# Performance work log

Hardware: AMD Instinct MI355X
Metric: run time of the kernel (lower is better)

The kernel has to match this reference:

```python
import jax, jax.numpy as jnp
import numpy as np

N, E, D_IN, D_OUT = 16384, 4096, 256, 256


def _leaky(v):
    return jnp.where(v > 0, v, 0.1 * v)


def setup_inputs() -> dict:
    key = jax.random.key(0)
    ks = jax.random.split(key, 8)
    x = jax.random.normal(ks[0], (N, D_IN), dtype=jnp.float32)
    # 0/1 incidence mask, float32 (as multiplied in the torch code)
    H_shape = jax.random.randint(ks[1], (N, E), 0, 2).astype(jnp.float32)
    w1 = jax.random.normal(ks[2], (D_IN, D_OUT), dtype=jnp.float32)
    w2 = jax.random.normal(ks[3], (D_OUT, D_OUT), dtype=jnp.float32)
    a1 = jax.random.normal(ks[4], (D_OUT, 1), dtype=jnp.float32)
    a21 = jax.random.normal(ks[5], (D_OUT, 1), dtype=jnp.float32)
    a22 = jax.random.normal(ks[6], (D_OUT, 1), dtype=jnp.float32)
    return {"x": x, "H_shape": H_shape, "w1": w1, "w2": w2,
            "a1": a1, "a21": a21, "a22": a22}


def reference(x, H_shape, w1, w2, a1, a21, a22):
    xw1 = x @ w1                                  # [N, D]
    # node->edge attention (masked softmax-like over nodes, axis -2)
    f = _leaky(xw1) @ a1                          # [N, 1]
    e = jnp.exp(jnp.tanh(f / 8) * 8) * H_shape    # [N, E]
    e = e / jnp.sum(e, axis=-2, keepdims=True)    # normalize over nodes
    # edge features
    f = _leaky(e.T @ xw1)                         # [E, D]
    # edge->node attention (masked normalize over edges, axis -1)
    b = (_leaky(f @ w2) @ a21).T + _leaky(xw1) @ a22  # [1,E] + [N,1] -> [N,E]
    b = jnp.exp(jnp.tanh(b / 8) * 8) * H_shape
    b = b / jnp.sum(b, axis=-1, keepdims=True)
    return _leaky(b @ f @ w2)                     # [N, D]
```

## Files before the change

### kernel.cpp

```cpp
#include <hip/hip_runtime.h>


typedef __attribute__((ext_vector_type(8))) short short8;
typedef __attribute__((ext_vector_type(4))) float f32x4;
typedef __attribute__((ext_vector_type(4))) int int4v;
typedef __attribute__((ext_vector_type(4))) unsigned int uint4v;

__device__ __forceinline__ float leakyf(float v) { return v > 0.f ? v : 0.1f * v; }
__device__ __forceinline__ float fastrcp(float x) { return __builtin_amdgcn_rcpf(x); }

__device__ __forceinline__ float satexpf(float t) {
    float u = fminf(fmaxf(t * 0.25f, -30.f), 30.f);
    float p = __expf(u);
    float th = (p - 1.f) * fastrcp(p + 1.f);
    return __expf(8.f * th);
}

__device__ __forceinline__ short f2b(float v) {
    unsigned int x = __float_as_uint(v);
    x += 0x7fffu + ((x >> 16) & 1u);
    return (short)(x >> 16);
}
__device__ __forceinline__ float b2f(short s) {
    return __uint_as_float(((unsigned int)(unsigned short)s) << 16);
}

__global__ __launch_bounds__(256) void transpose_split2(
        const float* __restrict__ s0, short* __restrict__ dh0, short* __restrict__ dl0,
        const float* __restrict__ s1, short* __restrict__ dh1, short* __restrict__ dl1) {
    const float* src = blockIdx.z ? s1 : s0;
    short* dh = blockIdx.z ? dh1 : dh0;
    short* dl = blockIdx.z ? dl1 : dl0;
    __shared__ float Ts[64][65];
    const int t = threadIdx.x;
    const long r0 = (long)blockIdx.x * 64;
    const long c0 = (long)blockIdx.y * 64;
    {
        const int row = t >> 2, cc = (t & 3) * 16;
        const float* p = src + (r0 + row) * 256 + c0 + cc;
#pragma unroll
        for (int i = 0; i < 4; ++i) {
            f32x4 v = *reinterpret_cast<const f32x4*>(p + i * 4);
#pragma unroll
            for (int k = 0; k < 4; ++k) Ts[row][cc + i * 4 + k] = v[k];
        }
    }
    __syncthreads();
    {
        const int cl = t >> 2, ch = (t & 3) * 16;
        short8 h0, h1, l0, l1;
#pragma unroll
        for (int i = 0; i < 8; ++i) {
            float v = Ts[ch + i][cl];
            short h = f2b(v);
            h0[i] = h; l0[i] = f2b(v - b2f(h));
        }
#pragma unroll
        for (int i = 0; i < 8; ++i) {
            float v = Ts[ch + 8 + i][cl];
            short h = f2b(v);
            h1[i] = h; l1[i] = f2b(v - b2f(h));
        }
        short* qh = dh + (c0 + cl) * 256 + r0 + ch;
        short* ql = dl + (c0 + cl) * 256 + r0 + ch;
        *reinterpret_cast<short8*>(qh) = h0;
        *reinterpret_cast<short8*>(qh + 8) = h1;
        *reinterpret_cast<short8*>(ql) = l0;
        *reinterpret_cast<short8*>(ql + 8) = l1;
    }
}

__global__ __launch_bounds__(256) void transposeH_pack(
        const float* __restrict__ H, char* __restrict__ HbT,
        unsigned int* __restrict__ Hbits) {
    __shared__ float Ts[64][65];
    const int t = threadIdx.x;
    const long r0 = (long)blockIdx.x * 64;
    const long c0 = (long)blockIdx.y * 64;
    {
        const int row = t >> 2, cc = (t & 3) * 16;
        const float* p = H + (r0 + row) * 4096L + c0 + cc;
#pragma unroll
        for (int i = 0; i < 4; ++i) {
            f32x4 v = *reinterpret_cast<const f32x4*>(p + i * 4);
#pragma unroll
            for (int k = 0; k < 4; ++k) Ts[row][cc + i * 4 + k] = v[k];
        }
    }
    __syncthreads();
    {
        const int cl = t >> 2, ch = (t & 3) * 16;
        uint4v pk;
#pragma unroll
        for (int wv = 0; wv < 4; ++wv) {
            unsigned int u = 0;
#pragma unroll
            for (int b = 0; b < 4; ++b)
                u |= (Ts[ch + wv * 4 + b][cl] != 0.f ? 1u : 0u) << (8 * b);
            pk[wv] = u;
        }
        *reinterpret_cast<uint4v*>(HbT + (c0 + cl) * 16384L + r0 + ch) = pk;
    }
    if (t < 128) {
        const int nl = t >> 1, w = t & 1;
        unsigned int u = 0;
#pragma unroll
        for (int b = 0; b < 32; ++b)
            u |= (Ts[nl][w * 32 + b] != 0.f ? 1u : 0u) << b;
        Hbits[(r0 + nl) * 128 + (c0 >> 5) + w] = u;
    }
}

__global__ __launch_bounds__(256) void gemm_xw1(
        const float* __restrict__ A, const short* __restrict__ Bh,
        const short* __restrict__ Bl, float* __restrict__ C) {
    __shared__ short Ash[128][72];
    __shared__ short Asl[128][72];
    __shared__ short Bsh[64][72];
    __shared__ short Bsl[64][72];
    const int t = threadIdx.x;
    const int wid = t >> 6, lane = t & 63;
    const int wm = wid & 1, wn = wid >> 1;
    const int quad = lane >> 4, l15 = lane & 15;
    const long m0 = (long)blockIdx.x * 128;
    const long n0 = (long)blockIdx.y * 64;
    f32x4 acc[4][2];
#pragma unroll
    for (int i = 0; i < 4; ++i)
#pragma unroll
        for (int j = 0; j < 2; ++j)
#pragma unroll
            for (int r = 0; r < 4; ++r) acc[i][j][r] = 0.f;

    for (int kb = 0; kb < 256; kb += 64) {
#pragma unroll
        for (int it = 0; it < 4; ++it) {
            const int cid = t + it * 256;
            const int row = cid >> 3, c8 = (cid & 7) * 8;
            const float* ap = A + (m0 + row) * 256 + kb + c8;
            f32x4 v0 = *reinterpret_cast<const f32x4*>(ap);
            f32x4 v1 = *reinterpret_cast<const f32x4*>(ap + 4);
            short8 hi, lo;
#pragma unroll
            for (int k = 0; k < 4; ++k) {
                short h0 = f2b(v0[k]); hi[k] = h0; lo[k] = f2b(v0[k] - b2f(h0));
                short h1 = f2b(v1[k]); hi[4 + k] = h1; lo[4 + k] = f2b(v1[k] - b2f(h1));
            }
            *reinterpret_cast<short8*>(&Ash[row][c8]) = hi;
            *reinterpret_cast<short8*>(&Asl[row][c8]) = lo;
        }
#pragma unroll
        for (int it = 0; it < 2; ++it) {
            const int cid = t + it * 256;
            const int row = cid >> 3, c8 = (cid & 7) * 8;
            *reinterpret_cast<short8*>(&Bsh[row][c8]) =
                *reinterpret_cast<const short8*>(Bh + (n0 + row) * 256 + kb + c8);
            *reinterpret_cast<short8*>(&Bsl[row][c8]) =
                *reinterpret_cast<const short8*>(Bl + (n0 + row) * 256 + kb + c8);
        }
        __syncthreads();
#pragma unroll
        for (int ks = 0; ks < 2; ++ks) {
            short8 ah[4], al[4], bh[2], bl[2];
#pragma unroll
            for (int i = 0; i < 4; ++i) {
                ah[i] = *reinterpret_cast<const short8*>(&Ash[wm * 64 + i * 16 + l15][ks * 32 + quad * 8]);
                al[i] = *reinterpret_cast<const short8*>(&Asl[wm * 64 + i * 16 + l15][ks * 32 + quad * 8]);
            }
#pragma unroll
            for (int j = 0; j < 2; ++j) {
                bh[j] = *reinterpret_cast<const short8*>(&Bsh[wn * 32 + j * 16 + l15][ks * 32 + quad * 8]);
                bl[j] = *reinterpret_cast<const short8*>(&Bsl[wn * 32 + j * 16 + l15][ks * 32 + quad * 8]);
            }
#pragma unroll
            for (int i = 0; i < 4; ++i)
#pragma unroll
                for (int j = 0; j < 2; ++j) {
                    acc[i][j] = __builtin_amdgcn_mfma_f32_16x16x32_bf16(ah[i], bh[j], acc[i][j], 0, 0, 0);
                    acc[i][j] = __builtin_amdgcn_mfma_f32_16x16x32_bf16(ah[i], bl[j], acc[i][j], 0, 0, 0);
                    acc[i][j] = __builtin_amdgcn_mfma_f32_16x16x32_bf16(al[i], bh[j], acc[i][j], 0, 0, 0);
                }
        }
        __syncthreads();
    }
#pragma unroll
    for (int i = 0; i < 4; ++i) {
        const long grow = m0 + wm * 64 + i * 16 + quad * 4;
#pragma unroll
        for (int j = 0; j < 2; ++j) {
            const long gcol = n0 + wn * 32 + j * 16 + l15;
#pragma unroll
            for (int r = 0; r < 4; ++r)
                C[(grow + r) * 256 + gcol] = acc[i][j][r];
        }
    }
}

__global__ __launch_bounds__(256) void node_stats1(
        const float* __restrict__ xw1, const float* __restrict__ a1,
        const float* __restrict__ a22, float* __restrict__ g_out,
        float* __restrict__ dn, unsigned int* __restrict__ ddmax) {
    __shared__ float Mx[4][260];
    const int t = threadIdx.x;
    const int n0 = blockIdx.x * 64;
    const int r = t >> 2, q = t & 3;
    const long n = n0 + r;
    const float* xp = xw1 + n * 256 + q * 64;
    float vals[64];
    float facc = 0.f, dacc = 0.f;
#pragma unroll
    for (int i = 0; i < 16; ++i) {
        f32x4 v  = *reinterpret_cast<const f32x4*>(xp + i * 4);
        f32x4 b1 = *reinterpret_cast<const f32x4*>(a1 + q * 64 + i * 4);
        f32x4 b2 = *reinterpret_cast<const f32x4*>(a22 + q * 64 + i * 4);
#pragma unroll
        for (int k = 0; k < 4; ++k) {
            float lv = leakyf(v[k]);
            facc += lv * b1[k];
            dacc += lv * b2[k];
            vals[i * 4 + k] = v[k];
        }
    }
    facc += __shfl_xor(facc, 1); facc += __shfl_xor(facc, 2);
    dacc += __shfl_xor(dacc, 1); dacc += __shfl_xor(dacc, 2);
    const float g = satexpf(facc);
    if (q == 0) { dn[n] = dacc; g_out[n] = g; }
    float lm[64];
#pragma unroll
    for (int i = 0; i < 64; ++i) lm[i] = fabsf(vals[i] * g);
#pragma unroll
    for (int m = 4; m < 64; m <<= 1)
#pragma unroll
        for (int i = 0; i < 64; ++i) lm[i] = fmaxf(lm[i], __shfl_xor(lm[i], m));
    float gm = g;
#pragma unroll
    for (int m = 1; m < 64; m <<= 1) gm = fmaxf(gm, __shfl_xor(gm, m));
    const int wv = t >> 6, lane = t & 63;
    if (lane < 4) {
#pragma unroll
        for (int i = 0; i < 64; ++i) Mx[wv][lane * 64 + i] = lm[i];
    }
    if (lane == 0) Mx[wv][256] = gm;
    __syncthreads();
    if (t < 256) {
        float m = fmaxf(fmaxf(Mx[0][t], Mx[1][t]), fmaxf(Mx[2][t], Mx[3][t]));
        atomicMax(&ddmax[t], __float_as_uint(m));
    }
    if (t == 0) {
        float m = fmaxf(fmaxf(Mx[0][256], Mx[1][256]), fmaxf(Mx[2][256], Mx[3][256]));
        atomicMax(&ddmax[256], __float_as_uint(m));
    }
}

__global__ __launch_bounds__(256) void quantize_y(
        const float* __restrict__ xw1, const float* __restrict__ g_in,
        const unsigned int* __restrict__ ddmax, char* __restrict__ yQ) {
    __shared__ unsigned int Qh[257][16];
    __shared__ unsigned int Ql[257][16];
    const int t = threadIdx.x;
    const int n0 = blockIdx.x * 64;
    const int dd0 = (t >> 4) * 16;
    const int w = t & 15;
    const int r4 = w * 4;
    float s[16];
#pragma unroll
    for (int i = 0; i < 16; ++i)
        s[i] = 32512.f / __uint_as_float(ddmax[dd0 + i]);
    const float sg = 32512.f / __uint_as_float(ddmax[256]);
    unsigned int bh[16], bl[16];
#pragma unroll
    for (int i = 0; i < 16; ++i) { bh[i] = 0u; bl[i] = 0u; }
    unsigned int gh = 0u, gl = 0u;
#pragma unroll
    for (int rr = 0; rr < 4; ++rr) {
        const long n = n0 + r4 + rr;
        const float gg = g_in[n];
        const float* xp = xw1 + n * 256 + dd0;
#pragma unroll
        for (int c = 0; c < 4; ++c) {
            f32x4 v = *reinterpret_cast<const f32x4*>(xp + c * 4);
#pragma unroll
            for (int k = 0; k < 4; ++k) {
                const int i = c * 4 + k;
                int qv = __float2int_rn(v[k] * gg * s[i]);
                qv = max(-32639, min(32639, qv));
                const int qh = (qv + 128) >> 8;
                const int ql = qv - (qh << 8);
                bh[i] |= ((unsigned int)(qh & 255)) << (8 * rr);
                bl[i] |= ((unsigned int)(ql & 255)) << (8 * rr);
            }
        }
        if (t < 16) {
            int qv = __float2int_rn(gg * sg);
            qv = max(-32639, min(32639, qv));
            const int qh = (qv + 128) >> 8;
            const int ql = qv - (qh << 8);
            gh |= ((unsigned int)(qh & 255)) << (8 * rr);
            gl |= ((unsigned int)(ql & 255)) << (8 * rr);
        }
    }
#pragma unroll
    for (int i = 0; i < 16; ++i) { Qh[dd0 + i][w] = bh[i]; Ql[dd0 + i][w] = bl[i]; }
    if (t < 16) { Qh[256][t] = gh; Ql[256][t] = gl; }
    __syncthreads();
#pragma unroll
    for (int it = 0; it < 2; ++it) {
        const int dd = it * 256 + t;
        if (dd < 288) {
#pragma unroll
            for (int s2 = 0; s2 < 4; ++s2) {
                uint4v vh, vl;
                if (dd < 257) {
                    vh = *reinterpret_cast<const uint4v*>(&Qh[dd][s2 * 4]);
                    vl = *reinterpret_cast<const uint4v*>(&Ql[dd][s2 * 4]);
                } else {
#pragma unroll
                    for (int k = 0; k < 4; ++k) { vh[k] = 0u; vl[k] = 0u; }
                }
                *reinterpret_cast<uint4v*>(yQ + (long)dd * 16384 + n0 + s2 * 16) = vh;
                *reinterpret_cast<uint4v*>(yQ + (long)(288 + dd) * 16384 + n0 + s2 * 16) = vl;
            }
        }
    }
}

__global__ __launch_bounds__(256) void gemm_c1_i8(
        const char* __restrict__ Ab, const char* __restrict__ Bb,
        float* __restrict__ Cp) {
    __shared__ char As[128][144];
    __shared__ char Bsh[96][144];
    __shared__ char Bsl[96][144];
    const int t = threadIdx.x;
    const int wid = t >> 6, lane = t & 63;
    const int wm = wid & 1, wn = wid >> 1;
    const int quad = lane >> 4, l15 = lane & 15;
    const long m0 = (long)blockIdx.x * 128;
    const long n0 = (long)blockIdx.y * 96;
    const long k0 = (long)blockIdx.z * 2048;
    float* Cz = Cp + (long)blockIdx.z * (4096L * 288);
    int4v acch[4][3], accl[4][3];
#pragma unroll
    for (int i = 0; i < 4; ++i)
#pragma unroll
        for (int j = 0; j < 3; ++j)
#pragma unroll
            for (int r = 0; r < 4; ++r) { acch[i][j][r] = 0; accl[i][j][r] = 0; }

    for (int kb = 0; kb < 2048; kb += 128) {
#pragma unroll
        for (int it = 0; it < 4; ++it) {
            const int cid = t + it * 256;
            const int row = cid >> 3, seg = (cid & 7) * 16;
            *reinterpret_cast<uint4v*>(&As[row][seg]) =
                *reinterpret_cast<const uint4v*>(Ab + (m0 + row) * 16384 + k0 + kb + seg);
        }
#pragma unroll
        for (int it = 0; it < 3; ++it) {
            const int cid = t + it * 256;
            const int row = cid >> 3, seg = (cid & 7) * 16;
            *reinterpret_cast<uint4v*>(&Bsh[row][seg]) =
                *reinterpret_cast<const uint4v*>(Bb + (n0 + row) * 16384 + k0 + kb + seg);
            *reinterpret_cast<uint4v*>(&Bsl[row][seg]) =
                *reinterpret_cast<const uint4v*>(Bb + (288 + n0 + row) * 16384 + k0 + kb + seg);
        }
        __syncthreads();
#pragma unroll
        for (int ks = 0; ks < 2; ++ks) {
            int4v af[4], bh[3], bl[3];
#pragma unroll
            for (int i = 0; i < 4; ++i)
                af[i] = *reinterpret_cast<const int4v*>(
                        &As[wm * 64 + i * 16 + l15][ks * 64 + quad * 16]);
#pragma unroll
            for (int j = 0; j < 3; ++j) {
                bh[j] = *reinterpret_cast<const int4v*>(
                        &Bsh[wn * 48 + j * 16 + l15][ks * 64 + quad * 16]);
                bl[j] = *reinterpret_cast<const int4v*>(
                        &Bsl[wn * 48 + j * 16 + l15][ks * 64 + quad * 16]);
            }
#pragma unroll
            for (int i = 0; i < 4; ++i)
#pragma unroll
                for (int j = 0; j < 3; ++j) {
                    acch[i][j] = __builtin_amdgcn_mfma_i32_16x16x64_i8(af[i], bh[j], acch[i][j], 0, 0, 0);
                    accl[i][j] = __builtin_amdgcn_mfma_i32_16x16x64_i8(af[i], bl[j], accl[i][j], 0, 0, 0);
                }
        }
        __syncthreads();
    }
#pragma unroll
    for (int i = 0; i < 4; ++i) {
        const long grow = m0 + wm * 64 + i * 16 + quad * 4;
#pragma unroll
        for (int j = 0; j < 3; ++j) {
            const long gcol = n0 + wn * 48 + j * 16 + l15;
#pragma unroll
            for (int r = 0; r < 4; ++r)
                Cz[(grow + r) * 288 + gcol] =
                    256.f * (float)acch[i][j][r] + (float)accl[i][j][r];
        }
    }
}

__global__ __launch_bounds__(256) void reduce_C1(
        const float* __restrict__ C1p, const unsigned int* __restrict__ ddmax,
        float* __restrict__ C1) {
    const int i = blockIdx.x * 256 + threadIdx.x;
    const int dd = i % 288;
    float s = 0.f;
#pragma unroll
    for (int z = 0; z < 8; ++z) s += C1p[(long)z * 4096 * 288 + i];
    C1[i] = s * (__uint_as_float(ddmax[dd]) * (1.f / 32512.f));
}

__global__ __launch_bounds__(256) void gemm_G(
        const float* __restrict__ C1, const short* __restrict__ w2Th,
        const short* __restrict__ w2Tl, const float* __restrict__ a21,
        short* __restrict__ GT, float* __restrict__ cat) {
    __shared__ short Ash[64][72];
    __shared__ short Asl[64][72];
    __shared__ short Bsh[64][72];
    __shared__ short Bsl[64][72];
    __shared__ float Gs[64][65];
    const int t = threadIdx.x;
    const int wid = t >> 6, lane = t & 63;
    const int wm = wid & 1, wn = wid >> 1;
    const int quad = lane >> 4, l15 = lane & 15;
    const long j0 = (long)blockIdx.x * 64;
    const long d0 = (long)blockIdx.y * 64;
    f32x4 acc[2][2];
#pragma unroll
    for (int i = 0; i < 2; ++i)
#pragma unroll
        for (int j = 0; j < 2; ++j)
#pragma unroll
            for (int r = 0; r < 4; ++r) acc[i][j][r] = 0.f;

    for (int kb = 0; kb < 256; kb += 64) {
#pragma unroll
        for (int it = 0; it < 2; ++it) {
            const int cid = t + it * 256;
            const int row = cid >> 3, c8 = (cid & 7) * 8;
            const float rd = fastrcp(C1[(j0 + row) * 288 + 256]);
            const float* ap = C1 + (j0 + row) * 288 + kb + c8;
            f32x4 v0 = *reinterpret_cast<const f32x4*>(ap);
            f32x4 v1 = *reinterpret_cast<const f32x4*>(ap + 4);
            short8 hi, lo;
#pragma unroll
            for (int k = 0; k < 4; ++k) {
                float f0 = leakyf(v0[k] * rd);
                float f1 = leakyf(v1[k] * rd);
                short h0 = f2b(f0); hi[k] = h0; lo[k] = f2b(f0 - b2f(h0));
                short h1 = f2b(f1); hi[4 + k] = h1; lo[4 + k] = f2b(f1 - b2f(h1));
            }
            *reinterpret_cast<short8*>(&Ash[row][c8]) = hi;
            *reinterpret_cast<short8*>(&Asl[row][c8]) = lo;
            *reinterpret_cast<short8*>(&Bsh[row][c8]) =
                *reinterpret_cast<const short8*>(w2Th + (d0 + row) * 256 + kb + c8);
            *reinterpret_cast<short8*>(&Bsl[row][c8]) =
                *reinterpret_cast<const short8*>(w2Tl + (d0 + row) * 256 + kb + c8);
        }
        __syncthreads();
#pragma unroll
        for (int ks = 0; ks < 2; ++ks) {
            short8 ah[2], al[2], bh[2], bl[2];
#pragma unroll
            for (int i = 0; i < 2; ++i) {
                ah[i] = *reinterpret_cast<const short8*>(&Ash[wm * 32 + i * 16 + l15][ks * 32 + quad * 8]);
                al[i] = *reinterpret_cast<const short8*>(&Asl[wm * 32 + i * 16 + l15][ks * 32 + quad * 8]);
            }
#pragma unroll
            for (int j = 0; j < 2; ++j) {
                bh[j] = *reinterpret_cast<const short8*>(&Bsh[wn * 32 + j * 16 + l15][ks * 32 + quad * 8]);
                bl[j] = *reinterpret_cast<const short8*>(&Bsl[wn * 32 + j * 16 + l15][ks * 32 + quad * 8]);
            }
#pragma unroll
            for (int i = 0; i < 2; ++i)
#pragma unroll
                for (int j = 0; j < 2; ++j) {
                    acc[i][j] = __builtin_amdgcn_mfma_f32_16x16x32_bf16(ah[i], bh[j], acc[i][j], 0, 0, 0);
                    acc[i][j] = __builtin_amdgcn_mfma_f32_16x16x32_bf16(ah[i], bl[j], acc[i][j], 0, 0, 0);
                    acc[i][j] = __builtin_amdgcn_mfma_f32_16x16x32_bf16(al[i], bh[j], acc[i][j], 0, 0, 0);
                }
        }
        __syncthreads();
    }
#pragma unroll
    for (int i = 0; i < 2; ++i)
#pragma unroll
        for (int j = 0; j < 2; ++j)
#pragma unroll
            for (int r = 0; r < 4; ++r)
                Gs[wm * 32 + i * 16 + quad * 4 + r][wn * 32 + j * 16 + l15] = acc[i][j][r];
    __syncthreads();
    {
        const int jl = t >> 2, q = t & 3;
        float cp = 0.f;
#pragma unroll
        for (int i = 0; i < 16; ++i) {
            const int d = q * 16 + i;
            cp += leakyf(Gs[jl][d]) * a21[d0 + d];
        }
        cp += __shfl_xor(cp, 1); cp += __shfl_xor(cp, 2);
        if (q == 0) atomicAdd(&cat[j0 + jl], cp);
    }
    {
        const int dl = t >> 2, q = t & 3;
        short8 pk0, pk1;
#pragma unroll
        for (int i = 0; i < 8; ++i) pk0[i] = f2b(Gs[q * 16 + i][dl]);
#pragma unroll
        for (int i = 0; i < 8; ++i) pk1[i] = f2b(Gs[q * 16 + 8 + i][dl]);
        short* gp = GT + (d0 + dl) * 4096 + j0 + q * 16;
        *reinterpret_cast<short8*>(gp) = pk0;
        *reinterpret_cast<short8*>(gp + 8) = pk1;
    }
}

__global__ __launch_bounds__(256) void fused_out(
        const unsigned int* __restrict__ Hbits, const float* __restrict__ cat,
        const float* __restrict__ dn, const short* __restrict__ GT,
        float* __restrict__ out) {
    __shared__ float catS[4096];
    __shared__ unsigned int bitsS[64][132];
    __shared__ short As[64][72];
    __shared__ short Bs[256][72];
    __shared__ float rsS[64][4];
    __shared__ float rinvS[64];
    const int t = threadIdx.x;
    const int wid = t >> 6, lane = t & 63;
    const int wm = wid & 1, wn = wid >> 1;
    const int quad = lane >> 4, l15 = lane & 15;
    const long m0 = (long)blockIdx.x * 64;
    const int r = t & 63, jc = t >> 6;
    const float drow = dn[m0 + r];

#pragma unroll
    for (int i = 0; i < 4; ++i) {
        f32x4 v = *reinterpret_cast<const f32x4*>(cat + t * 16 + i * 4);
        *reinterpret_cast<f32x4*>(&catS[t * 16 + i * 4]) = v;
    }
#pragma unroll
    for (int it = 0; it < 8; ++it) {
        const int cid = t + it * 256;
        const int row = cid >> 5, ch = (cid & 31) * 4;
        *reinterpret_cast<uint4v*>(&bitsS[row][ch]) =
            *reinterpret_cast<const uint4v*>(Hbits + (m0 + row) * 128 + ch);
    }

    f32x4 acc[2][8];
#pragma unroll
    for (int i = 0; i < 2; ++i)
#pragma unroll
        for (int j = 0; j < 8; ++j)
#pragma unroll
            for (int x = 0; x < 4; ++x) acc[i][j][x] = 0.f;
    float racc = 0.f;
    __syncthreads();

    for (int kb = 0; kb < 4096; kb += 64) {
#pragma unroll
        for (int it = 0; it < 8; ++it) {
            const int cid = t + it * 256;
            const int row = cid >> 3, c8 = (cid & 7) * 8;
            *reinterpret_cast<short8*>(&Bs[row][c8]) =
                *reinterpret_cast<const short8*>(GT + row * 4096 + kb + c8);
        }
        {
            const unsigned int w = bitsS[r][(kb >> 5) + (jc >> 1)];
            const int bo = (jc & 1) * 16;
            short8 pk0, pk1;
#pragma unroll
            for (int c = 0; c < 4; ++c) {
                f32x4 cv = *reinterpret_cast<const f32x4*>(&catS[kb + jc * 16 + c * 4]);
#pragma unroll
                for (int k = 0; k < 4; ++k) {
                    const int kk = c * 4 + k;
                    const float s = ((w >> (bo + kk)) & 1u) ? satexpf(cv[k] + drow) : 0.f;
                    const short sb = f2b(s);
                    if (kk < 8) pk0[kk] = sb; else pk1[kk - 8] = sb;
                    racc += b2f(sb);
                }
            }
            *reinterpret_cast<short8*>(&As[r][jc * 16]) = pk0;
            *reinterpret_cast<short8*>(&As[r][jc * 16 + 8]) = pk1;
        }
        __syncthreads();
#pragma unroll
        for (int ks = 0; ks < 2; ++ks) {
            short8 af[2], bf[8];
#pragma unroll
            for (int i = 0; i < 2; ++i)
                af[i] = *reinterpret_cast<const short8*>(
                        &As[wm * 32 + i * 16 + l15][ks * 32 + quad * 8]);
#pragma unroll
            for (int j = 0; j < 8; ++j)
                bf[j] = *reinterpret_cast<const short8*>(
                        &Bs[wn * 128 + j * 16 + l15][ks * 32 + quad * 8]);
#pragma unroll
            for (int i = 0; i < 2; ++i)
#pragma unroll
                for (int j = 0; j < 8; ++j)
                    acc[i][j] = __builtin_amdgcn_mfma_f32_16x16x32_bf16(
                            af[i], bf[j], acc[i][j], 0, 0, 0);
        }
        __syncthreads();
    }
    rsS[r][jc] = racc;
    __syncthreads();
    if (t < 64)
        rinvS[t] = fastrcp(rsS[t][0] + rsS[t][1] + rsS[t][2] + rsS[t][3]);
    __syncthreads();
#pragma unroll
    for (int i = 0; i < 2; ++i) {
#pragma unroll
        for (int j = 0; j < 8; ++j) {
            const long gcol = wn * 128 + j * 16 + l15;
#pragma unroll
            for (int x = 0; x < 4; ++x) {
                const int rl = wm * 32 + i * 16 + quad * 4 + x;
                out[(m0 + rl) * 256 + gcol] = leakyf(acc[i][j][x] * rinvS[rl]);
            }
        }
    }
}

extern "C" void kernel_launch(void* const* d_in, const int* in_sizes, int n_in,
                              void* d_out, int out_size, void* d_ws, size_t ws_size,
                              hipStream_t stream) {
    const float* x   = (const float*)d_in[0];
    const float* H   = (const float*)d_in[1];
    const float* w1  = (const float*)d_in[2];
    const float* w2  = (const float*)d_in[3];
    const float* a1  = (const float*)d_in[4];
    const float* a21 = (const float*)d_in[5];
    const float* a22 = (const float*)d_in[6];
    float* out = (float*)d_out;
    char* ws = (char*)d_ws;

    float* xw1   = (float*)(ws + 0);
    float* C1p   = (float*)(ws + 0);
    char*  HbT   = (char*)(ws + 67108864);
    char*  yQ    = (char*)(ws + 134217728);
    float* dn    = (float*)(ws + 143654912);
    float* g     = (float*)(ws + 143720448);
    unsigned int* ddmax = (unsigned int*)(ws + 143785984);
    short* w1Th  = (short*)(ws + 143790080);
    short* w1Tl  = (short*)(ws + 143921152);
    short* w2Th  = (short*)(ws + 144052224);
    short* w2Tl  = (short*)(ws + 144183296);
    float* C1    = (float*)(ws + 144314368);
    short* GT    = (short*)(ws + 149032960);
    float* cat   = (float*)(ws + 151130112);
    unsigned int* Hbits = (unsigned int*)(ws + 151212032);

    hipMemsetAsync(ddmax, 0, 288 * sizeof(unsigned int), stream);
    hipMemsetAsync(cat, 0, 4096 * sizeof(float), stream);

    transpose_split2<<<dim3(4, 4, 2), 256, 0, stream>>>(
            w1, w1Th, w1Tl, w2, w2Th, w2Tl);
    transposeH_pack<<<dim3(256, 64), 256, 0, stream>>>(H, HbT, Hbits);

    gemm_xw1<<<dim3(128, 4), 256, 0, stream>>>(x, w1Th, w1Tl, xw1);
    node_stats1<<<dim3(256), 256, 0, stream>>>(xw1, a1, a22, g, dn, ddmax);
    quantize_y<<<dim3(256), 256, 0, stream>>>(xw1, g, ddmax, yQ);

    gemm_c1_i8<<<dim3(32, 3, 8), 256, 0, stream>>>(HbT, yQ, C1p);
    reduce_C1<<<dim3(4608), 256, 0, stream>>>(C1p, ddmax, C1);

    gemm_G<<<dim3(64, 4), 256, 0, stream>>>(C1, w2Th, w2Tl, a21, GT, cat);

    fused_out<<<dim3(256), 256, 0, stream>>>(Hbits, cat, dn, GT, out);
}
```

Baseline: 682.5 us.

## Store transposed incidence as bits and expand to int8 in C1 GEMM; widen fused_out

The transpose kernel now writes a bit-packed transposed incidence matrix instead of the 64 MB byte matrix. The int8 C1 GEMM reads these bits and expands them to 0/1 bytes in shared memory with a multiply-mask trick. It also changes the tile shape to 256x48 with split-K of 4, which halves the partial-sum reduction. fused_out moves to 512 threads, drops the shared cat and bits staging, and reads cat and bit words directly from global memory. This cuts the incidence write and read traffic by 8x, in exchange for extra ALU work on bit expansion and fewer parallel blocks in the C1 GEMM.

Result: no change. 675.6 us (-1.0%).

```diff
diff --git a/kernel.cpp b/kernel.cpp
--- a/kernel.cpp
+++ b/kernel.cpp
@@ -23,6 +23,9 @@
 }
 __device__ __forceinline__ float b2f(short s) {
     return __uint_as_float(((unsigned int)(unsigned short)s) << 16);
+}
+__device__ __forceinline__ unsigned int bits4_to_bytes(unsigned int s) {
+    return ((s & 0xFu) * 0x00204081u) & 0x01010101u;
 }
 
 __global__ __launch_bounds__(256) void transpose_split2(
@@ -71,8 +74,8 @@
 }
 
 __global__ __launch_bounds__(256) void transposeH_pack(
-        const float* __restrict__ H, char* __restrict__ HbT,
-        unsigned int* __restrict__ Hbits) {
+        const float* __restrict__ H, unsigned int* __restrict__ Hbits,
+        unsigned int* __restrict__ HbitsT) {
     __shared__ float Ts[64][65];
     const int t = threadIdx.x;
     const long r0 = (long)blockIdx.x * 64;
@@ -88,19 +91,6 @@
         }
     }
     __syncthreads();
-    {
-        const int cl = t >> 2, ch = (t & 3) * 16;
-        uint4v pk;
-#pragma unroll
-        for (int wv = 0; wv < 4; ++wv) {
-            unsigned int u = 0;
-#pragma unroll
-            for (int b = 0; b < 4; ++b)
-                u |= (Ts[ch + wv * 4 + b][cl] != 0.f ? 1u : 0u) << (8 * b);
-            pk[wv] = u;
-        }
-        *reinterpret_cast<uint4v*>(HbT + (c0 + cl) * 16384L + r0 + ch) = pk;
-    }
     if (t < 128) {
         const int nl = t >> 1, w = t & 1;
         unsigned int u = 0;
@@ -108,6 +98,14 @@
         for (int b = 0; b < 32; ++b)
             u |= (Ts[nl][w * 32 + b] != 0.f ? 1u : 0u) << b;
         Hbits[(r0 + nl) * 128 + (c0 >> 5) + w] = u;
+    } else {
+        const int t2 = t - 128;
+        const int jl = t2 >> 1, w = t2 & 1;
+        unsigned int u = 0;
+#pragma unroll
+        for (int b = 0; b < 32; ++b)
+            u |= (Ts[w * 32 + b][jl] != 0.f ? 1u : 0u) << b;
+        HbitsT[(c0 + jl) * 512 + (r0 >> 5) + w] = u;
     }
 }
 
@@ -324,19 +322,18 @@
     }
 }
 
-__global__ __launch_bounds__(256) void gemm_c1_i8(
-        const char* __restrict__ Ab, const char* __restrict__ Bb,
+__global__ __launch_bounds__(256) void gemm_c1_bits(
+        const unsigned int* __restrict__ HbitsT, const char* __restrict__ Bb,
         float* __restrict__ Cp) {
-    __shared__ char As[128][144];
-    __shared__ char Bsh[96][144];
-    __shared__ char Bsl[96][144];
+    __shared__ char As[256][144];
+    __shared__ char Bsh[48][144];
+    __shared__ char Bsl[48][144];
     const int t = threadIdx.x;
     const int wid = t >> 6, lane = t & 63;
-    const int wm = wid & 1, wn = wid >> 1;
     const int quad = lane >> 4, l15 = lane & 15;
-    const long m0 = (long)blockIdx.x * 128;
-    const long n0 = (long)blockIdx.y * 96;
-    const long k0 = (long)blockIdx.z * 2048;
+    const long m0 = (long)blockIdx.x * 256;
+    const long n0 = (long)blockIdx.y * 48;
+    const long k0 = (long)blockIdx.z * 4096;
     float* Cz = Cp + (long)blockIdx.z * (4096L * 288);
     int4v acch[4][3], accl[4][3];
 #pragma unroll
@@ -346,22 +343,31 @@
 #pragma unroll
             for (int r = 0; r < 4; ++r) { acch[i][j][r] = 0; accl[i][j][r] = 0; }
 
-    for (int kb = 0; kb < 2048; kb += 128) {
-#pragma unroll
-        for (int it = 0; it < 4; ++it) {
-            const int cid = t + it * 256;
-            const int row = cid >> 3, seg = (cid & 7) * 16;
-            *reinterpret_cast<uint4v*>(&As[row][seg]) =
-                *reinterpret_cast<const uint4v*>(Ab + (m0 + row) * 16384 + k0 + kb + seg);
+    for (int kb = 0; kb < 4096; kb += 128) {
+        {
+            uint4v bv = *reinterpret_cast<const uint4v*>(
+                    HbitsT + (m0 + t) * 512 + ((k0 + kb) >> 5));
+#pragma unroll
+            for (int w4 = 0; w4 < 4; ++w4) {
+                const unsigned int u = bv[w4];
+                uint4v e0, e1;
+#pragma unroll
+                for (int k = 0; k < 4; ++k) e0[k] = bits4_to_bytes(u >> (4 * k));
+#pragma unroll
+                for (int k = 0; k < 4; ++k) e1[k] = bits4_to_bytes(u >> (16 + 4 * k));
+                *reinterpret_cast<uint4v*>(&As[t][w4 * 32]) = e0;
+                *reinterpret_cast<uint4v*>(&As[t][w4 * 32 + 16]) = e1;
+            }
         }
 #pragma unroll
         for (int it = 0; it < 3; ++it) {
             const int cid = t + it * 256;
-            const int row = cid >> 3, seg = (cid & 7) * 16;
-            *reinterpret_cast<uint4v*>(&Bsh[row][seg]) =
-                *reinterpret_cast<const uint4v*>(Bb + (n0 + row) * 16384 + k0 + kb + seg);
-            *reinterpret_cast<uint4v*>(&Bsl[row][seg]) =
-                *reinterpret_cast<const uint4v*>(Bb + (288 + n0 + row) * 16384 + k0 + kb + seg);
+            const int idx = (cid < 384) ? cid : cid - 384;
+            const int row = idx >> 3, seg = (idx & 7) * 16;
+            char* dst = (cid >= 384) ? &Bsl[row][seg] : &Bsh[row][seg];
+            const long srow = (cid >= 384) ? (288 + n0 + row) : (n0 + row);
+            *reinterpret_cast<uint4v*>(dst) =
+                *reinterpret_cast<const uint4v*>(Bb + srow * 16384 + k0 + kb + seg);
         }
         __syncthreads();
 #pragma unroll
@@ -370,13 +376,11 @@
 #pragma unroll
             for (int i = 0; i < 4; ++i)
                 af[i] = *reinterpret_cast<const int4v*>(
-                        &As[wm * 64 + i * 16 + l15][ks * 64 + quad * 16]);
+                        &As[wid * 64 + i * 16 + l15][ks * 64 + quad * 16]);
 #pragma unroll
             for (int j = 0; j < 3; ++j) {
-                bh[j] = *reinterpret_cast<const int4v*>(
-                        &Bsh[wn * 48 + j * 16 + l15][ks * 64 + quad * 16]);
-                bl[j] = *reinterpret_cast<const int4v*>(
-                        &Bsl[wn * 48 + j * 16 + l15][ks * 64 + quad * 16]);
+                bh[j] = *reinterpret_cast<const int4v*>(&Bsh[j * 16 + l15][ks * 64 + quad * 16]);
+                bl[j] = *reinterpret_cast<const int4v*>(&Bsl[j * 16 + l15][ks * 64 + quad * 16]);
             }
 #pragma unroll
             for (int i = 0; i < 4; ++i)
@@ -390,10 +394,10 @@
     }
 #pragma unroll
     for (int i = 0; i < 4; ++i) {
-        const long grow = m0 + wm * 64 + i * 16 + quad * 4;
+        const long grow = m0 + wid * 64 + i * 16 + quad * 4;
 #pragma unroll
         for (int j = 0; j < 3; ++j) {
-            const long gcol = n0 + wn * 48 + j * 16 + l15;
+            const long gcol = n0 + j * 16 + l15;
 #pragma unroll
             for (int r = 0; r < 4; ++r)
                 Cz[(grow + r) * 288 + gcol] =
@@ -409,7 +413,7 @@
     const int dd = i % 288;
     float s = 0.f;
 #pragma unroll
-    for (int z = 0; z < 8; ++z) s += C1p[(long)z * 4096 * 288 + i];
+    for (int z = 0; z < 4; ++z) s += C1p[(long)z * 4096 * 288 + i];
     C1[i] = s * (__uint_as_float(ddmax[dd]) * (1.f / 32512.f));
 }
 
@@ -517,105 +521,97 @@
     }
 }
 
-__global__ __launch_bounds__(256) void fused_out(
+__global__ __launch_bounds__(512) void fused_out(
         const unsigned int* __restrict__ Hbits, const float* __restrict__ cat,
         const float* __restrict__ dn, const short* __restrict__ GT,
         float* __restrict__ out) {
-    __shared__ float catS[4096];
-    __shared__ unsigned int bitsS[64][132];
     __shared__ short As[64][72];
     __shared__ short Bs[256][72];
-    __shared__ float rsS[64][4];
+    __shared__ float rsS[64][8];
     __shared__ float rinvS[64];
     const int t = threadIdx.x;
     const int wid = t >> 6, lane = t & 63;
-    const int wm = wid & 1, wn = wid >> 1;
+    const int wm = wid >> 2, wn = wid & 3;
     const int quad = lane >> 4, l15 = lane & 15;
     const long m0 = (long)blockIdx.x * 64;
-    const int r = t & 63, jc = t >> 6;
+    const int r = lane, jc8 = wid;
     const float drow = dn[m0 + r];
-
-#pragma unroll
-    for (int i = 0; i < 4; ++i) {
-        f32x4 v = *reinterpret_cast<const f32x4*>(cat + t * 16 + i * 4);
-        *reinterpret_cast<f32x4*>(&catS[t * 16 + i * 4]) = v;
-    }
-#pragma unroll
-    for (int it = 0; it < 8; ++it) {
-        const int cid = t + it * 256;
-        const int row = cid >> 5, ch = (cid & 31) * 4;
-        *reinterpret_cast<uint4v*>(&bitsS[row][ch]) =
-            *reinterpret_cast<const uint4v*>(Hbits + (m0 + row) * 128 + ch);
-    }
-
-    f32x4 acc[2][8];
+    const int bc = jc8 >> 2;
+    const int bo = (jc8 & 3) * 8;
+
+    f32x4 acc[2][4];
 #pragma unroll
     for (int i = 0; i < 2; ++i)
 #pragma unroll
-        for (int j = 0; j < 8; ++j)
+        for (int j = 0; j < 4; ++j)
 #pragma unroll
             for (int x = 0; x < 4; ++x) acc[i][j][x] = 0.f;
     float racc = 0.f;
-    __syncthreads();
-
-    for (int kb = 0; kb < 4096; kb += 64) {
-#pragma unroll
-        for (int it = 0; it < 8; ++it) {
-            const int cid = t + it * 256;
-            const int row = cid >> 3, c8 = (cid & 7) * 8;
-            *reinterpret_cast<short8*>(&Bs[row][c8]) =
-                *reinterpret_cast<const short8*>(GT + row * 4096 + kb + c8);
-        }
-        {
-            const unsigned int w = bitsS[r][(kb >> 5) + (jc >> 1)];
-            const int bo = (jc & 1) * 16;
-            short8 pk0, pk1;
-#pragma unroll
-            for (int c = 0; c < 4; ++c) {
-                f32x4 cv = *reinterpret_cast<const f32x4*>(&catS[kb + jc * 16 + c * 4]);
-#pragma unroll
-                for (int k = 0; k < 4; ++k) {
-                    const int kk = c * 4 + k;
-                    const float s = ((w >> (bo + kk)) & 1u) ? satexpf(cv[k] + drow) : 0.f;
+
+    for (int kb2 = 0; kb2 < 4096; kb2 += 128) {
+        const uint4v bw = *reinterpret_cast<const uint4v*>(
+                Hbits + (m0 + r) * 128 + (kb2 >> 5));
+#pragma unroll
+        for (int half = 0; half < 2; ++half) {
+            const int kb = kb2 + half * 64;
+#pragma unroll
+            for (int it = 0; it < 4; ++it) {
+                const int cid = t + it * 512;
+                const int row = cid >> 3, c8 = (cid & 7) * 8;
+                *reinterpret_cast<short8*>(&Bs[row][c8]) =
+                    *reinterpret_cast<const short8*>(GT + row * 4096 + kb + c8);
+            }
+            {
+                const unsigned int w = bw[half * 2 + bc];
+                f32x4 cv0 = *reinterpret_cast<const f32x4*>(cat + kb + jc8 * 8);
+                f32x4 cv1 = *reinterpret_cast<const f32x4*>(cat + kb + jc8 * 8 + 4);
+                short8 pk;
+#pragma unroll
+                for (int k = 0; k < 8; ++k) {
+                    const float cvk = (k < 4) ? cv0[k & 3] : cv1[k & 3];
+                    const float s = ((w >> (bo + k)) & 1u) ? satexpf(cvk + drow) : 0.f;
                     const short sb = f2b(s);
-                    if (kk < 8) pk0[kk] = sb; else pk1[kk - 8] = sb;
+                    pk[k] = sb;
                     racc += b2f(sb);
                 }
-            }
-            *reinterpret_cast<short8*>(&As[r][jc * 16]) = pk0;
-            *reinterpret_cast<short8*>(&As[r][jc * 16 + 8]) = pk1;
-        }
-        __syncthreads();
-#pragma unroll
-        for (int ks = 0; ks < 2; ++ks) {
-            short8 af[2], bf[8];
-#pragma unroll
-            for (int i = 0; i < 2; ++i)
-                af[i] = *reinterpret_cast<const short8*>(
-                        &As[wm * 32 + i * 16 + l15][ks * 32 + quad * 8]);
-#pragma unroll
-            for (int j = 0; j < 8; ++j)
-                bf[j] = *reinterpret_cast<const short8*>(
-                        &Bs[wn * 128 + j * 16 + l15][ks * 32 + quad * 8]);
-#pragma unroll
-            for (int i = 0; i < 2; ++i)
-#pragma unroll
-                for (int j = 0; j < 8; ++j)
-                    acc[i][j] = __builtin_amdgcn_mfma_f32_16x16x32_bf16(
-                            af[i], bf[j], acc[i][j], 0, 0, 0);
-        }
-        __syncthreads();
-    }
-    rsS[r][jc] = racc;
+                *reinterpret_cast<short8*>(&As[r][jc8 * 8]) = pk;
+            }
+            __syncthreads();
+#pragma unroll
+            for (int ks = 0; ks < 2; ++ks) {
+                short8 af[2], bf[4];
+#pragma unroll
+                for (int i = 0; i < 2; ++i)
+                    af[i] = *reinterpret_cast<const short8*>(
+                            &As[wm * 32 + i * 16 + l15][ks * 32 + quad * 8]);
+#pragma unroll
+                for (int j = 0; j < 4; ++j)
+                    bf[j] = *reinterpret_cast<const short8*>(
+                            &Bs[wn * 64 + j * 16 + l15][ks * 32 + quad * 8]);
+#pragma unroll
+                for (int i = 0; i < 2; ++i)
+#pragma unroll
+                    for (int j = 0; j < 4; ++j)
+                        acc[i][j] = __builtin_amdgcn_mfma_f32_16x16x32_bf16(
+                                af[i], bf[j], acc[i][j], 0, 0, 0);
+            }
+            __syncthreads();
+        }
+    }
+    rsS[r][jc8] = racc;
     __syncthreads();
-    if (t < 64)
-        rinvS[t] = fastrcp(rsS[t][0] + rsS[t][1] + rsS[t][2] + rsS[t][3]);
+    if (t < 64) {
+        float s = 0.f;
+#pragma unroll
+        for (int i = 0; i < 8; ++i) s += rsS[t][i];
+        rinvS[t] = fastrcp(s);
+    }
     __syncthreads();
 #pragma unroll
     for (int i = 0; i < 2; ++i) {
 #pragma unroll
-        for (int j = 0; j < 8; ++j) {
-            const long gcol = wn * 128 + j * 16 + l15;
+        for (int j = 0; j < 4; ++j) {
+            const long gcol = wn * 64 + j * 16 + l15;
 #pragma unroll
             for (int x = 0; x < 4; ++x) {
                 const int rl = wm * 32 + i * 16 + quad * 4 + x;
@@ -640,35 +636,35 @@
 
     float* xw1   = (float*)(ws + 0);
     float* C1p   = (float*)(ws + 0);
-    char*  HbT   = (char*)(ws + 67108864);
-    char*  yQ    = (char*)(ws + 134217728);
-    float* dn    = (float*)(ws + 143654912);
-    float* g     = (float*)(ws + 143720448);
-    unsigned int* ddmax = (unsigned int*)(ws + 143785984);
-    short* w1Th  = (short*)(ws + 143790080);
-    short* w1Tl  = (short*)(ws + 143921152);
-    short* w2Th  = (short*)(ws + 144052224);
-    short* w2Tl  = (short*)(ws + 144183296);
-    float* C1    = (float*)(ws + 144314368);
-    short* GT    = (short*)(ws + 149032960);
-    float* cat   = (float*)(ws + 151130112);
-    unsigned int* Hbits = (unsigned int*)(ws + 151212032);
+    char*  yQ    = (char*)(ws + 67108864);
+    float* dn    = (float*)(ws + 76546048);
+    float* g     = (float*)(ws + 76611584);
+    unsigned int* ddmax = (unsigned int*)(ws + 76677120);
+    short* w1Th  = (short*)(ws + 76681216);
+    short* w1Tl  = (short*)(ws + 76812288);
+    short* w2Th  = (short*)(ws + 76943360);
+    short* w2Tl  = (short*)(ws + 77074432);
+    float* C1    = (float*)(ws + 77205504);
+    short* GT    = (short*)(ws + 81924096);
+    float* cat   = (float*)(ws + 84021248);
+    unsigned int* Hbits  = (unsigned int*)(ws + 84037632);
+    unsigned int* HbitsT = (unsigned int*)(ws + 92426240);
 
     hipMemsetAsync(ddmax, 0, 288 * sizeof(unsigned int), stream);
     hipMemsetAsync(cat, 0, 4096 * sizeof(float), stream);
 
     transpose_split2<<<dim3(4, 4, 2), 256, 0, stream>>>(
             w1, w1Th, w1Tl, w2, w2Th, w2Tl);
-    transposeH_pack<<<dim3(256, 64), 256, 0, stream>>>(H, HbT, Hbits);
+    transposeH_pack<<<dim3(256, 64), 256, 0, stream>>>(H, Hbits, HbitsT);
 
     gemm_xw1<<<dim3(128, 4), 256, 0, stream>>>(x, w1Th, w1Tl, xw1);
     node_stats1<<<dim3(256), 256, 0, stream>>>(xw1, a1, a22, g, dn, ddmax);
     quantize_y<<<dim3(256), 256, 0, stream>>>(xw1, g, ddmax, yQ);
 
-    gemm_c1_i8<<<dim3(32, 3, 8), 256, 0, stream>>>(HbT, yQ, C1p);
+    gemm_c1_bits<<<dim3(16, 6, 4), 256, 0, stream>>>(HbitsT, yQ, C1p);
     reduce_C1<<<dim3(4608), 256, 0, stream>>>(C1p, ddmax, C1);
 
     gemm_G<<<dim3(64, 4), 256, 0, stream>>>(C1, w2Th, w2Tl, a21, GT, cat);
 
-    fused_out<<<dim3(256), 256, 0, stream>>>(Hbits, cat, dn, GT, out);
-}
+    fused_out<<<dim3(256), 512, 0, stream>>>(Hbits, cat, dn, GT, out);
+}
```
